# Kernel optimization log

Measured on AMD Instinct MI355X. Metric: run time of the kernel, lower is better.

The kernel has to match this reference:

```python
import jax, jax.numpy as jnp
import numpy as np

B, S, H = 32, 256, 1024   # batch, seq_len, xlmr hidden
HL = 512                  # lstm hidden per direction
E = 256                   # entity_feature_size
L = 5                     # languages: en fr de es it
LN_EPS = 1e-5


def setup_inputs() -> dict:
    key = jax.random.key(0)
    ks = jax.random.split(key, 12)
    sc = 0.02
    sequence_output = jax.random.normal(ks[0], (B, S, H), jnp.float32)
    lengths = jax.random.randint(ks[1], (B,), S // 2, S + 1)
    attention_mask = (jnp.arange(S)[None, :] < lengths[:, None]).astype(jnp.int32)
    language_ids = jax.random.randint(ks[2], (B,), 0, L).astype(jnp.int64)
    # per-language adapter params (stacked over lang dim)
    W1 = jax.random.normal(ks[3], (L, H, H), jnp.float32) * sc
    b1 = jnp.zeros((L, H), jnp.float32)
    ln_g = jnp.ones((L, H), jnp.float32)
    ln_b = jnp.zeros((L, H), jnp.float32)
    W2 = jax.random.normal(ks[4], (L, H, H), jnp.float32) * sc
    b2 = jnp.zeros((L, H), jnp.float32)
    # BiLSTM params, torch gate order (i, f, g, o); b = b_ih + b_hh
    Wih_f = jax.random.normal(ks[5], (4 * HL, H), jnp.float32) * sc
    Whh_f = jax.random.normal(ks[6], (4 * HL, HL), jnp.float32) * sc
    b_f = jnp.zeros((4 * HL,), jnp.float32)
    Wih_b = jax.random.normal(ks[7], (4 * HL, H), jnp.float32) * sc
    Whh_b = jax.random.normal(ks[8], (4 * HL, HL), jnp.float32) * sc
    b_b = jnp.zeros((4 * HL,), jnp.float32)
    # projection 2*HL -> E
    Wp = jax.random.normal(ks[9], (E, 2 * HL), jnp.float32) * sc
    bp = jnp.zeros((E,), jnp.float32)
    return dict(sequence_output=sequence_output, attention_mask=attention_mask,
                language_ids=language_ids, W1=W1, b1=b1, ln_g=ln_g, ln_b=ln_b,
                W2=W2, b2=b2, Wih_f=Wih_f, Whh_f=Whh_f, b_f=b_f,
                Wih_b=Wih_b, Whh_b=Whh_b, b_b=b_b, Wp=Wp, bp=bp)


def _lstm_scan(x, mask, Wih, Whh, b):
    """x: [S,B,H], mask: [S,B,1] bool. Returns hidden states [S,B,HL].
    Masked steps keep state and emit 0 (pack/pad_packed semantics)."""
    h0 = jnp.zeros((x.shape[1], Whh.shape[1]), x.dtype)

    def step(carry, inp):
        h, c = carry
        x_t, m = inp
        gates = x_t @ Wih.T + h @ Whh.T + b
        i, f, g, o = jnp.split(gates, 4, axis=-1)
        c_new = jax.nn.sigmoid(f) * c + jax.nn.sigmoid(i) * jnp.tanh(g)
        h_new = jax.nn.sigmoid(o) * jnp.tanh(c_new)
        h = jnp.where(m, h_new, h)
        c = jnp.where(m, c_new, c)
        return (h, c), jnp.where(m, h_new, 0.0)

    _, ys = jax.lax.scan(step, (h0, h0), (x, mask))
    return ys


def reference(sequence_output, attention_mask, language_ids, W1, b1, ln_g, ln_b,
              W2, b2, Wih_f, Whh_f, b_f, Wih_b, Whh_b, b_b, Wp, bp):
    # --- all 5 language adapters on the full batch, then masked-sum ---
    h = jnp.einsum('bsh,lhd->lbsd', sequence_output, W1) + b1[:, None, None, :]
    mu = h.mean(-1, keepdims=True)
    var = h.var(-1, keepdims=True)
    h = (h - mu) * jax.lax.rsqrt(var + LN_EPS) * ln_g[:, None, None, :] + ln_b[:, None, None, :]
    h = jax.nn.relu(h)
    h = jnp.einsum('lbsd,ldh->lbsh', h, W2) + b2[:, None, None, :]
    onehot = jax.nn.one_hot(language_ids, L, dtype=h.dtype)          # [B,L]
    adapted = jnp.einsum('lbsh,bl->bsh', h, onehot)                  # [B,S,H]
    # --- BiLSTM over valid lengths (packed-sequence semantics) ---
    x = adapted.transpose(1, 0, 2)                                    # [S,B,H]
    m = attention_mask.astype(bool).T[:, :, None]                     # [S,B,1]
    ys_f = _lstm_scan(x, m, Wih_f, Whh_f, b_f)                        # [S,B,HL]
    ys_b = _lstm_scan(x[::-1], m[::-1], Wih_b, Whh_b, b_b)[::-1]      # [S,B,HL]
    lstm_out = jnp.concatenate([ys_f, ys_b], -1).transpose(1, 0, 2)   # [B,S,2HL]
    return lstm_out @ Wp.T + bp                                       # [B,S,E]
```

## Files before the change

kernel.cpp:

```cpp
#include <hip/hip_runtime.h>

typedef __bf16 bft;
typedef bft bf16x8 __attribute__((ext_vector_type(8)));
typedef bft bf16x4 __attribute__((ext_vector_type(4)));
typedef bft bf16x2 __attribute__((ext_vector_type(2)));
typedef float f32x4 __attribute__((ext_vector_type(4)));
typedef unsigned long long u64;
typedef unsigned int u32;
typedef u32 u32x4 __attribute__((ext_vector_type(4)));

#define LN_EPS 1e-5f


__device__ __forceinline__ float sigmoidf_(float x) {
    return 1.f / (1.f + __expf(-x));
}
__device__ __forceinline__ float tanhf_(float x) {
    float e = __expf(-2.f * fabsf(x));
    float t = (1.f - e) / (1.f + e);
    return copysignf(t, x);
}

__global__ void cvt_f32_bf16(const float* __restrict__ in, bft* __restrict__ out, int n4) {
    int i = blockIdx.x * blockDim.x + threadIdx.x;
    if (i < n4) {
        float4 v = ((const float4*)in)[i];
        bf16x4 o = { (bft)v.x, (bft)v.y, (bft)v.z, (bft)v.w };
        ((bf16x4*)out)[i] = o;
    }
}

__global__ void zero_u32(u32* __restrict__ p, int n) {
    int i = blockIdx.x * blockDim.x + threadIdx.x;
    if (i < n) p[i] = 0u;
}

__global__ void pack_mask(const int* __restrict__ mask, u32* __restrict__ mbits) {
    int t = blockIdx.x * blockDim.x + threadIdx.x;
    if (t < 256) {
        int w = t >> 5, b = t & 31;
        u32 v = 0;
        for (int i = 0; i < 32; ++i)
            v |= (mask[b * 256 + w * 32 + i] ? 1u : 0u) << i;
        mbits[w * 32 + b] = v;
    }
}

__global__ __launch_bounds__(256) void cvt_permute_wih(
    const float* __restrict__ in, bft* __restrict__ out)
{
    int r = blockIdx.x;
    int src = (r & 3) * 512 + (r >> 2);
    int t = threadIdx.x;
    float4 v = ((const float4*)(in + (size_t)src * 1024))[t];
    bf16x4 o = { (bft)v.x, (bft)v.y, (bft)v.z, (bft)v.w };
    ((bf16x4*)(out + (size_t)r * 1024))[t] = o;
}

__global__ void permute_bias(const float* __restrict__ in, float* __restrict__ out) {
    int t = blockIdx.x * blockDim.x + threadIdx.x;
    if (t < 2048) out[t] = in[(t & 3) * 512 + (t >> 2)];
}

__global__ __launch_bounds__(256) void transpose_cvt_w(
    const float* __restrict__ W1, const float* __restrict__ W2,
    bft* __restrict__ W1t, bft* __restrict__ W2t)
{
    __shared__ float tile[32][33];
    int z = blockIdx.z;
    int l = z >> 1;
    const float* src = ((z & 1) ? W2 : W1) + ((size_t)l << 20);
    bft* dst = ((z & 1) ? W2t : W1t) + ((size_t)l << 20);
    int tx = threadIdx.x & 31, ty = threadIdx.x >> 5;
    int bx = blockIdx.x * 32, by = blockIdx.y * 32;
    for (int r = ty; r < 32; r += 8)
        tile[r][tx] = src[(size_t)(by + r) * 1024 + bx + tx];
    __syncthreads();
    for (int r = ty; r < 32; r += 8)
        dst[(size_t)(bx + r) * 1024 + by + tx] = (bft)tile[tx][r];
}

__global__ __launch_bounds__(256) void gemm_bt(
    const bft* __restrict__ A, const bft* __restrict__ Bt,
    const float* __restrict__ bias, const int* __restrict__ langs,
    int langStrideB, int langStrideBias,
    float* __restrict__ outF, bft* __restrict__ outB,
    int remapLog, int remapMul, int ldc)
{
    const int K = 1024;
    int tn = blockIdx.x, tm = blockIdx.y;
    int row0 = tm * 128, col0 = tn * 128;
    int lang = langs ? langs[row0 >> 8] : 0;
    const bft* Ap = A + (size_t)row0 * K;
    const bft* Bp = Bt + (size_t)lang * langStrideB + (size_t)col0 * K;
    const float* biasp = bias + (size_t)lang * langStrideBias + col0;

    __shared__ bft As[128 * 32];
    __shared__ bft Bs[128 * 32];

    int t = threadIdx.x;
    int lane = t & 63, wave = t >> 6;
    int wm = wave & 1, wn = wave >> 1;
    int lrow = lane & 15, quad = lane >> 4;

    f32x4 acc[4][4] = {};

    for (int k0 = 0; k0 < K; k0 += 32) {
        __syncthreads();
        for (int c = t; c < 512; c += 256) {
            int r = c >> 2, co = (c & 3) << 3;
            *(uint4*)(As + r * 32 + co) = *(const uint4*)(Ap + (size_t)r * K + k0 + co);
            *(uint4*)(Bs + r * 32 + co) = *(const uint4*)(Bp + (size_t)r * K + k0 + co);
        }
        __syncthreads();
        bf16x8 af[4], bfr[4];
#pragma unroll
        for (int i = 0; i < 4; ++i)
            af[i] = *(const bf16x8*)(As + (wm * 64 + i * 16 + lrow) * 32 + quad * 8);
#pragma unroll
        for (int j = 0; j < 4; ++j)
            bfr[j] = *(const bf16x8*)(Bs + (wn * 64 + j * 16 + lrow) * 32 + quad * 8);
#pragma unroll
        for (int i = 0; i < 4; ++i)
#pragma unroll
            for (int j = 0; j < 4; ++j)
                acc[i][j] = __builtin_amdgcn_mfma_f32_16x16x32_bf16(af[i], bfr[j], acc[i][j], 0, 0, 0);
    }

#pragma unroll
    for (int i = 0; i < 4; ++i) {
#pragma unroll
        for (int j = 0; j < 4; ++j) {
#pragma unroll
            for (int r = 0; r < 4; ++r) {
                int m = wm * 64 + i * 16 + quad * 4 + r;
                int n = wn * 64 + j * 16 + lrow;
                int grow = row0 + m;
                float v = acc[i][j][r] + biasp[n];
                size_t idx;
                if (remapLog < 0) {
                    int b = grow >> 8, s = grow & 255;
                    int col = col0 + n;
                    int jj = col >> 2, gg = col & 3;
                    int jp = jj & 7, gs = jj >> 3;
                    int tc = (((b >> 4) * 2 + (jp >> 2)) << 6) + ((jp & 3) << 4) + (b & 15);
                    idx = (((size_t)s * 64 + gs) << 10) + (tc << 2) + gg;
                } else {
                    int orow = remapLog ? ((grow & ((1 << remapLog) - 1)) * remapMul + (grow >> remapLog))
                                        : grow;
                    idx = (size_t)orow * ldc + col0 + n;
                }
                if (outF) outF[idx] = v;
                else outB[idx] = (bft)v;
            }
        }
    }
}

__global__ __launch_bounds__(256) void ln_relu_kernel(
    const float* __restrict__ h1, bft* __restrict__ a2,
    const float* __restrict__ ln_g, const float* __restrict__ ln_b,
    const int* __restrict__ langs)
{
    int row = blockIdx.x;
    int lang = langs[row >> 8];
    const float* x = h1 + (size_t)row * 1024;
    int t = threadIdx.x;
    float4 v = ((const float4*)x)[t];
    float s = v.x + v.y + v.z + v.w;
    float ss = v.x * v.x + v.y * v.y + v.z * v.z + v.w * v.w;
#pragma unroll
    for (int off = 32; off > 0; off >>= 1) {
        s += __shfl_down(s, off, 64);
        ss += __shfl_down(ss, off, 64);
    }
    __shared__ float red[8];
    int wave = t >> 6, lane = t & 63;
    if (lane == 0) { red[wave] = s; red[4 + wave] = ss; }
    __syncthreads();
    float S = red[0] + red[1] + red[2] + red[3];
    float SS = red[4] + red[5] + red[6] + red[7];
    float mean = S * (1.f / 1024.f);
    float var = SS * (1.f / 1024.f) - mean * mean;
    float inv = rsqrtf(var + LN_EPS);
    float4 g = ((const float4*)(ln_g + (size_t)lang * 1024))[t];
    float4 b = ((const float4*)(ln_b + (size_t)lang * 1024))[t];
    float y0 = fmaxf(0.f, (v.x - mean) * inv * g.x + b.x);
    float y1 = fmaxf(0.f, (v.y - mean) * inv * g.y + b.y);
    float y2 = fmaxf(0.f, (v.z - mean) * inv * g.z + b.z);
    float y3 = fmaxf(0.f, (v.w - mean) * inv * g.w + b.w);
    bf16x4 o = { (bft)y0, (bft)y1, (bft)y2, (bft)y3 };
    ((bf16x4*)(a2 + (size_t)row * 1024))[t] = o;
}

__global__ __launch_bounds__(256) void bilstm_kernel(
    const bft* __restrict__ gin_f, const bft* __restrict__ gin_b,
    const bft* __restrict__ Whh_f, const bft* __restrict__ Whh_b,
    const u32* __restrict__ mbits, bft* __restrict__ ys,
    u32* __restrict__ hg, u32* __restrict__ ctr)
{
    __shared__ u64 smem[4096];
    bft* hs  = (bft*)smem;
    u32* hsd = (u32*)smem;

    int blk = blockIdx.x;
    int dir = blk >> 6;
    int gslice = blk & 63;
    int jbase = gslice << 3;
    const bft* Whh = dir ? Whh_b : Whh_f;
    const bft* gin = dir ? gin_b : gin_f;

    int t = threadIdx.x;
    int lane = t & 63, wave = t >> 6;
    int wm = wave & 1, wn = wave >> 1;
    int lrow = lane & 15, quad = lane >> 4;

    bf16x8 wf[16];
    {
        int row32 = wm * 16 + lrow;
        int jl = row32 >> 2, g = row32 & 3;
        const bft* wp = Whh + (size_t)(g * 512 + jbase + jl) * 512 + quad * 8;
#pragma unroll
        for (int kk = 0; kk < 16; ++kk)
            wf[kk] = *(const bf16x8*)(wp + kk * 32);
    }

    int batch = wn * 16 + lrow;
    u32* ysU = (u32*)ys;
    float cs = 0.f, hp = 0.f;
    u32 mw = 0;

    for (int it = 0; it < 256; ++it) {
        int tt = dir ? (255 - it) : it;

        bf16x4 gv = *(const bf16x4*)(gin + ((((size_t)tt * 64 + gslice) << 10) + (t << 2)));
        if ((it & 31) == 0) mw = mbits[(tt >> 5) * 32 + batch];
        int mk = (mw >> (tt & 31)) & 1;

        if (it == 0) {
#pragma unroll
            for (int i = 0; i < 16; ++i)
                smem[t + i * 256] = 0ull;
        } else {
            if (wave == 0) {
                u32 c = 8u;
                const u32* cp = ctr + ((size_t)(dir * 256 + it) * 32 + (lane & 31)) * 16;
                for (;;) {
                    if (lane < 32)
                        c = __hip_atomic_load(cp, __ATOMIC_RELAXED, __HIP_MEMORY_SCOPE_AGENT);
                    if (__all(c >= 8u)) break;
                    __builtin_amdgcn_s_sleep(1);
                }
            }
            __syncthreads();
            const u32* hq = hg + (size_t)(dir * 2 + (it & 1)) * 8192;
            u32x4 r[8];
#pragma unroll
            for (int i = 0; i < 8; ++i)
                asm volatile("global_load_dwordx4 %0, %1, off sc0 sc1"
                             : "=v"(r[i]) : "v"(hq + i * 1024 + t * 4) : "memory");
            asm volatile("s_waitcnt vmcnt(0)" ::: "memory");
#pragma unroll
            for (int i = 0; i < 8; ++i) {
                int bat = t & 31, gs = i * 8 + (t >> 5);
                *(u32x4*)(hsd + bat * 256 + ((gs ^ (bat & 7)) << 2)) = r[i];
            }
        }
        __syncthreads();

        f32x4 acc0 = {}, acc1 = {};
#pragma unroll
        for (int kk = 0; kk < 16; ++kk) {
            int b16 = kk * 4 + quad;
            bf16x8 b = *(const bf16x8*)(hs + batch * 512 + ((b16 ^ (batch & 7)) << 3));
            if (kk & 1) acc1 = __builtin_amdgcn_mfma_f32_16x16x32_bf16(wf[kk], b, acc1, 0, 0, 0);
            else        acc0 = __builtin_amdgcn_mfma_f32_16x16x32_bf16(wf[kk], b, acc0, 0, 0, 0);
        }
        f32x4 acc = acc0 + acc1;

        float xi = acc[0] + (float)gv[0];
        float xf = acc[1] + (float)gv[1];
        float xg = acc[2] + (float)gv[2];
        float xo = acc[3] + (float)gv[3];
        float cn = sigmoidf_(xf) * cs + sigmoidf_(xi) * tanhf_(xg);
        float hn = sigmoidf_(xo) * tanhf_(cn);
        if (mk) { cs = cn; hp = hn; }
        union { bft h; unsigned short u; } hc; hc.h = (bft)hp;
        u32 own = (u32)hc.u | ((mk ? (u32)hc.u : 0u) << 16);
        u32 par = __shfl_xor(own, 16, 64);
        u32 hpair = (own & 0xffffu) | (par << 16);
        u32 ypair = (own >> 16) | (par & 0xffff0000u);

        if (!(lane & 16)) {
            u32* ha = hg + (size_t)(dir * 2 + ((it + 1) & 1)) * 8192
                         + gslice * 128 + batch * 4 + wm * 2 + (quad >> 1);
            asm volatile("global_store_dword %0, %1, off sc0 sc1" :: "v"(ha), "v"(hpair) : "memory");
        }
        asm volatile("s_waitcnt vmcnt(0)" ::: "memory");
        if (lane == 0 && it < 255)
            __hip_atomic_fetch_add(ctr + ((size_t)(dir * 256 + it + 1) * 32
                                          + (gslice & 7) * 4 + wave) * 16,
                                   1u, __ATOMIC_RELAXED, __HIP_MEMORY_SCOPE_AGENT);
        if (!(lane & 16))
            ysU[((size_t)tt * 32 + batch) * 512 + dir * 256
                + (jbase >> 1) + wm * 2 + (quad >> 1)] = ypair;
    }
}

extern "C" void kernel_launch(void* const* d_in, const int* in_sizes, int n_in,
                              void* d_out, int out_size, void* d_ws, size_t ws_size,
                              hipStream_t stream)
{
    const float* X     = (const float*)d_in[0];
    const int*   amask = (const int*)d_in[1];
    const int*   langs = (const int*)d_in[2];
    const float* W1    = (const float*)d_in[3];
    const float* b1    = (const float*)d_in[4];
    const float* ln_g  = (const float*)d_in[5];
    const float* ln_b  = (const float*)d_in[6];
    const float* W2    = (const float*)d_in[7];
    const float* b2    = (const float*)d_in[8];
    const float* Wih_f = (const float*)d_in[9];
    const float* Whh_f = (const float*)d_in[10];
    const float* b_f   = (const float*)d_in[11];
    const float* Wih_b = (const float*)d_in[12];
    const float* Whh_b = (const float*)d_in[13];
    const float* b_b   = (const float*)d_in[14];
    const float* Wp    = (const float*)d_in[15];
    const float* bp    = (const float*)d_in[16];
    float* out = (float*)d_out;

    char* ws = (char*)d_ws;
    size_t off = 0;
    auto alloc = [&](size_t bytes) -> void* {
        void* p = ws + off;
        off += (bytes + 255) & ~(size_t)255;
        return p;
    };
    bft* Xbf   = (bft*)alloc(8192ull * 1024 * 2);
    bft* W1t   = (bft*)alloc(5ull * 1024 * 1024 * 2);
    bft* W2t   = (bft*)alloc(5ull * 1024 * 1024 * 2);
    bft* Wihf  = (bft*)alloc(2048ull * 1024 * 2);
    bft* Wihb  = (bft*)alloc(2048ull * 1024 * 2);
    bft* Whhf  = (bft*)alloc(2048ull * 512 * 2);
    bft* Whhb  = (bft*)alloc(2048ull * 512 * 2);
    bft* Wpb   = (bft*)alloc(256ull * 1024 * 2);
    float* h1  = (float*)alloc(8192ull * 1024 * 4);
    bft* a2    = (bft*)alloc(8192ull * 1024 * 2);
    bft* adapt = (bft*)alloc(8192ull * 1024 * 2);
    bft* ginf  = (bft*)alloc(256ull * 32 * 2048 * 2);
    bft* ginb  = (bft*)alloc(256ull * 32 * 2048 * 2);
    bft* ysb   = (bft*)alloc(256ull * 32 * 1024 * 2);
    float* pbf = (float*)alloc(2048ull * 4);
    float* pbb = (float*)alloc(2048ull * 4);
    u32* hg    = (u32*)alloc(2ull * 2 * 64 * 32 * 4 * 4);
    u32* ctr   = (u32*)alloc(2ull * 256 * 32 * 16 * 4);
    u32* mbits = (u32*)alloc(256ull * 4);
    (void)ws_size; (void)in_sizes; (void)n_in; (void)out_size;

    auto cvt = [&](const float* src, bft* dst, int n) {
        int n4 = n >> 2;
        hipLaunchKernelGGL(cvt_f32_bf16, dim3((n4 + 255) / 256), dim3(256), 0, stream, src, dst, n4);
    };
    cvt(X, Xbf, 8192 * 1024);
    hipLaunchKernelGGL(cvt_permute_wih, dim3(2048), dim3(256), 0, stream, Wih_f, Wihf);
    hipLaunchKernelGGL(cvt_permute_wih, dim3(2048), dim3(256), 0, stream, Wih_b, Wihb);
    cvt(Whh_f, Whhf, 2048 * 512);
    cvt(Whh_b, Whhb, 2048 * 512);
    cvt(Wp, Wpb, 256 * 1024);
    hipLaunchKernelGGL(permute_bias, dim3(8), dim3(256), 0, stream, b_f, pbf);
    hipLaunchKernelGGL(permute_bias, dim3(8), dim3(256), 0, stream, b_b, pbb);
    hipLaunchKernelGGL(zero_u32, dim3(1024), dim3(256), 0, stream, ctr, 262144);
    hipLaunchKernelGGL(pack_mask, dim3(1), dim3(256), 0, stream, amask, mbits);
    hipLaunchKernelGGL(transpose_cvt_w, dim3(32, 32, 10), dim3(256), 0, stream, W1, W2, W1t, W2t);

    hipLaunchKernelGGL(gemm_bt, dim3(8, 64), dim3(256), 0, stream,
        Xbf, W1t, b1, langs, 1024 * 1024, 1024, h1, (bft*)nullptr, 0, 0, 1024);
    hipLaunchKernelGGL(ln_relu_kernel, dim3(8192), dim3(256), 0, stream, h1, a2, ln_g, ln_b, langs);
    hipLaunchKernelGGL(gemm_bt, dim3(8, 64), dim3(256), 0, stream,
        a2, W2t, b2, langs, 1024 * 1024, 1024, (float*)nullptr, adapt, 0, 0, 1024);
    hipLaunchKernelGGL(gemm_bt, dim3(16, 64), dim3(256), 0, stream,
        adapt, Wihf, pbf, (const int*)nullptr, 0, 0, (float*)nullptr, ginf, -1, 0, 0);
    hipLaunchKernelGGL(gemm_bt, dim3(16, 64), dim3(256), 0, stream,
        adapt, Wihb, pbb, (const int*)nullptr, 0, 0, (float*)nullptr, ginb, -1, 0, 0);
    {
        void* args[] = { (void*)&ginf, (void*)&ginb, (void*)&Whhf, (void*)&Whhb,
                         (void*)&mbits, (void*)&ysb, (void*)&hg, (void*)&ctr };
        hipLaunchCooperativeKernel((const void*)bilstm_kernel, dim3(128), dim3(256), args, 0, stream);
    }
    hipLaunchKernelGGL(gemm_bt, dim3(2, 64), dim3(256), 0, stream,
        ysb, Wpb, bp, (const int*)nullptr, 0, 0, out, (bft*)nullptr, 5, 256, 256);
}
```

Measured before the change: 1.305 ms.

## Replace counter-based grid barrier in BiLSTM with sentinel-flagged hidden-state buffers

```diff
diff --git a/kernel.cpp b/kernel.cpp
--- a/kernel.cpp
+++ b/kernel.cpp
@@ -10,6 +10,7 @@
 typedef u32 u32x4 __attribute__((ext_vector_type(4)));
 
 #define LN_EPS 1e-5f
+#define SENT 0x7FC17FC1u
 
 
 __device__ __forceinline__ float sigmoidf_(float x) {
@@ -30,9 +31,10 @@
     }
 }
 
-__global__ void zero_u32(u32* __restrict__ p, int n) {
+__global__ void init_hg(u32* __restrict__ hg) {
     int i = blockIdx.x * blockDim.x + threadIdx.x;
-    if (i < n) p[i] = 0u;
+    int buf = (i >> 13) & 3;
+    hg[i] = (buf == 0) ? 0u : SENT;
 }
 
 __global__ void pack_mask(const int* __restrict__ mask, u32* __restrict__ mbits) {
@@ -197,7 +199,7 @@
     const bft* __restrict__ gin_f, const bft* __restrict__ gin_b,
     const bft* __restrict__ Whh_f, const bft* __restrict__ Whh_b,
     const u32* __restrict__ mbits, bft* __restrict__ ys,
-    u32* __restrict__ hg, u32* __restrict__ ctr)
+    u32* __restrict__ hg)
 {
     __shared__ u64 smem[4096];
     bft* hs  = (bft*)smem;
@@ -206,9 +208,9 @@
     int blk = blockIdx.x;
     int dir = blk >> 6;
     int gslice = blk & 63;
-    int jbase = gslice << 3;
     const bft* Whh = dir ? Whh_b : Whh_f;
     const bft* gin = dir ? gin_b : gin_f;
+    u32* hbase = hg + (size_t)dir * 4 * 8192;
 
     int t = threadIdx.x;
     int lane = t & 63, wave = t >> 6;
@@ -219,7 +221,7 @@
     {
         int row32 = wm * 16 + lrow;
         int jl = row32 >> 2, g = row32 & 3;
-        const bft* wp = Whh + (size_t)(g * 512 + jbase + jl) * 512 + quad * 8;
+        const bft* wp = Whh + (size_t)(g * 512 + (gslice << 3) + jl) * 512 + quad * 8;
 #pragma unroll
         for (int kk = 0; kk < 16; ++kk)
             wf[kk] = *(const bf16x8*)(wp + kk * 32);
@@ -237,34 +239,38 @@
         if ((it & 31) == 0) mw = mbits[(tt >> 5) * 32 + batch];
         int mk = (mw >> (tt & 31)) & 1;
 
-        if (it == 0) {
-#pragma unroll
-            for (int i = 0; i < 16; ++i)
-                smem[t + i * 256] = 0ull;
-        } else {
-            if (wave == 0) {
-                u32 c = 8u;
-                const u32* cp = ctr + ((size_t)(dir * 256 + it) * 32 + (lane & 31)) * 16;
-                for (;;) {
-                    if (lane < 32)
-                        c = __hip_atomic_load(cp, __ATOMIC_RELAXED, __HIP_MEMORY_SCOPE_AGENT);
-                    if (__all(c >= 8u)) break;
-                    __builtin_amdgcn_s_sleep(1);
-                }
-            }
-            __syncthreads();
-            const u32* hq = hg + (size_t)(dir * 2 + (it & 1)) * 8192;
-            u32x4 r[8];
+        if (!(lane & 16)) {
+            u32* ca = hbase + (size_t)((it + 2) & 3) * 8192
+                            + gslice * 128 + batch * 4 + wm * 2 + (quad >> 1);
+            u32 sv = SENT;
+            asm volatile("global_store_dword %0, %1, off sc0 sc1" :: "v"(ca), "v"(sv) : "memory");
+        }
+
+        __syncthreads();
+
+        const u32* hq = hbase + (size_t)(it & 3) * 8192;
+        u32x4 r[8];
+        u32 need = 0xffu;
+        for (;;) {
 #pragma unroll
             for (int i = 0; i < 8; ++i)
-                asm volatile("global_load_dwordx4 %0, %1, off sc0 sc1"
-                             : "=v"(r[i]) : "v"(hq + i * 1024 + t * 4) : "memory");
+                if (need & (1u << i))
+                    asm volatile("global_load_dwordx4 %0, %1, off sc0 sc1"
+                                 : "=v"(r[i]) : "v"(hq + i * 1024 + t * 4) : "memory");
             asm volatile("s_waitcnt vmcnt(0)" ::: "memory");
 #pragma unroll
-            for (int i = 0; i < 8; ++i) {
-                int bat = t & 31, gs = i * 8 + (t >> 5);
-                *(u32x4*)(hsd + bat * 256 + ((gs ^ (bat & 7)) << 2)) = r[i];
-            }
+            for (int i = 0; i < 8; ++i)
+                if ((need & (1u << i)) &&
+                    r[i][0] != SENT && r[i][1] != SENT && r[i][2] != SENT && r[i][3] != SENT)
+                    need &= ~(1u << i);
+            if (!need) break;
+            __builtin_amdgcn_s_sleep(2);
+        }
+
+#pragma unroll
+        for (int i = 0; i < 8; ++i) {
+            int bat = t & 31, gs = i * 8 + (t >> 5);
+            *(u32x4*)(hsd + bat * 256 + ((gs ^ (bat & 7)) << 2)) = r[i];
         }
         __syncthreads();
 
@@ -292,18 +298,12 @@
         u32 ypair = (own >> 16) | (par & 0xffff0000u);
 
         if (!(lane & 16)) {
-            u32* ha = hg + (size_t)(dir * 2 + ((it + 1) & 1)) * 8192
-                         + gslice * 128 + batch * 4 + wm * 2 + (quad >> 1);
+            u32* ha = hbase + (size_t)((it + 1) & 3) * 8192
+                            + gslice * 128 + batch * 4 + wm * 2 + (quad >> 1);
             asm volatile("global_store_dword %0, %1, off sc0 sc1" :: "v"(ha), "v"(hpair) : "memory");
-        }
-        asm volatile("s_waitcnt vmcnt(0)" ::: "memory");
-        if (lane == 0 && it < 255)
-            __hip_atomic_fetch_add(ctr + ((size_t)(dir * 256 + it + 1) * 32
-                                          + (gslice & 7) * 4 + wave) * 16,
-                                   1u, __ATOMIC_RELAXED, __HIP_MEMORY_SCOPE_AGENT);
-        if (!(lane & 16))
             ysU[((size_t)tt * 32 + batch) * 512 + dir * 256
-                + (jbase >> 1) + wm * 2 + (quad >> 1)] = ypair;
+                + (gslice << 2) + wm * 2 + (quad >> 1)] = ypair;
+        }
     }
 }
 
@@ -353,8 +353,7 @@
     bft* ysb   = (bft*)alloc(256ull * 32 * 1024 * 2);
     float* pbf = (float*)alloc(2048ull * 4);
     float* pbb = (float*)alloc(2048ull * 4);
-    u32* hg    = (u32*)alloc(2ull * 2 * 64 * 32 * 4 * 4);
-    u32* ctr   = (u32*)alloc(2ull * 256 * 32 * 16 * 4);
+    u32* hg    = (u32*)alloc(2ull * 4 * 8192 * 4);
     u32* mbits = (u32*)alloc(256ull * 4);
     (void)ws_size; (void)in_sizes; (void)n_in; (void)out_size;
 
@@ -370,7 +369,7 @@
     cvt(Wp, Wpb, 256 * 1024);
     hipLaunchKernelGGL(permute_bias, dim3(8), dim3(256), 0, stream, b_f, pbf);
     hipLaunchKernelGGL(permute_bias, dim3(8), dim3(256), 0, stream, b_b, pbb);
-    hipLaunchKernelGGL(zero_u32, dim3(1024), dim3(256), 0, stream, ctr, 262144);
+    hipLaunchKernelGGL(init_hg, dim3(256), dim3(256), 0, stream, hg);
     hipLaunchKernelGGL(pack_mask, dim3(1), dim3(256), 0, stream, amask, mbits);
     hipLaunchKernelGGL(transpose_cvt_w, dim3(32, 32, 10), dim3(256), 0, stream, W1, W2, W1t, W2t);
 
@@ -385,7 +384,7 @@
         adapt, Wihb, pbb, (const int*)nullptr, 0, 0, (float*)nullptr, ginb, -1, 0, 0);
     {
         void* args[] = { (void*)&ginf, (void*)&ginb, (void*)&Whhf, (void*)&Whhb,
-                         (void*)&mbits, (void*)&ysb, (void*)&hg, (void*)&ctr };
+                         (void*)&mbits, (void*)&ysb, (void*)&hg };
         hipLaunchCooperativeKernel((const void*)bilstm_kernel, dim3(128), dim3(256), args, 0, stream);
     }
     hipLaunchKernelGGL(gemm_bt, dim3(2, 64), dim3(256), 0, stream,
```

Result: faster. 1.276 ms (-2.2%).
